# Performance work log

Hardware: AMD Instinct MI355X
Metric: run time of the kernel (lower is better)

Reference implementation:

```python
import jax, jax.numpy as jnp
import numpy as np

B, N, D_MODEL, HEADS, DFF, M = 4, 4096, 1024, 16, 4096, 256
DH = D_MODEL // HEADS  # 64
EPS_K = 1e-4
LN_EPS = 1e-5


def setup_inputs() -> dict:
    key = jax.random.key(0)
    ks = jax.random.split(key, 12)
    s = 0.02
    return {
        "video": jax.random.normal(ks[0], (B, N, D_MODEL), jnp.float32),
        "Wq": jax.random.normal(ks[1], (D_MODEL, D_MODEL), jnp.float32) * s,
        "bq": jnp.zeros((D_MODEL,), jnp.float32),
        "Wk": jax.random.normal(ks[2], (D_MODEL, D_MODEL), jnp.float32) * s,
        "bk": jnp.zeros((D_MODEL,), jnp.float32),
        "Wv": jax.random.normal(ks[3], (D_MODEL, D_MODEL), jnp.float32) * s,
        "bv": jnp.zeros((D_MODEL,), jnp.float32),
        "Wo": jax.random.normal(ks[4], (D_MODEL, D_MODEL), jnp.float32) * s,
        "bo": jnp.zeros((D_MODEL,), jnp.float32),
        "proj": jax.random.normal(ks[5], (M, DH), jnp.float32),  # random-feature matrix (buffer)
        "W1": jax.random.normal(ks[6], (DFF, D_MODEL), jnp.float32) * s,
        "b1": jnp.zeros((DFF,), jnp.float32),
        "W2": jax.random.normal(ks[7], (D_MODEL, DFF), jnp.float32) * s,
        "b2": jnp.zeros((D_MODEL,), jnp.float32),
        "g2": jnp.ones((D_MODEL,), jnp.float32),
        "be2": jnp.zeros((D_MODEL,), jnp.float32),
        "g3": jnp.ones((D_MODEL,), jnp.float32),
        "be3": jnp.zeros((D_MODEL,), jnp.float32),
    }


def softmax_kernel(x, proj, is_query):
    # FAVOR+ positive softmax random features (Performer).
    # x: [b,h,n,dh], proj: [m,dh]
    norm = x.shape[-1] ** -0.25  # data normalizer 1/d^{1/4}
    ratio = proj.shape[0] ** -0.5
    xp = jnp.einsum("bhnd,md->bhnm", x * norm, proj)
    diag = jnp.sum(jnp.square(x), axis=-1, keepdims=True) * 0.5 * (norm * norm)
    if is_query:
        stab = jnp.max(xp, axis=-1, keepdims=True)
    else:
        stab = jnp.max(xp, axis=(-1, -2), keepdims=True)
    return ratio * (jnp.exp(xp - diag - stab) + EPS_K)


def layer_norm(x, g, b):
    mu = jnp.mean(x, axis=-1, keepdims=True)
    var = jnp.mean(jnp.square(x - mu), axis=-1, keepdims=True)
    return (x - mu) * jax.lax.rsqrt(var + LN_EPS) * g + b


def reference(video, Wq, bq, Wk, bk, Wv, bv, Wo, bo, proj,
              W1, b1, W2, b2, g2, be2, g3, be3):
    b, n, d = video.shape
    split = lambda t: t.reshape(b, n, HEADS, DH).transpose(0, 2, 1, 3)  # [b,h,n,dh]
    q = split(video @ Wq.T + bq)
    k = split(video @ Wk.T + bk)
    v = split(video @ Wv.T + bv)

    qp = softmax_kernel(q, proj, is_query=True)   # [b,h,n,m]
    kp = softmax_kernel(k, proj, is_query=False)  # [b,h,n,m]

    # Non-causal linear attention: O(n*m*dh) instead of O(n^2)
    k_sum = jnp.sum(kp, axis=2)                              # [b,h,m]
    denom = jnp.einsum("bhnm,bhm->bhn", qp, k_sum)           # [b,h,n]
    ctx = jnp.einsum("bhnm,bhnd->bhmd", kp, v)               # [b,h,m,dh]
    out = jnp.einsum("bhnm,bhmd->bhnd", qp, ctx) / denom[..., None]

    attn = out.transpose(0, 2, 1, 3).reshape(b, n, d) @ Wo.T + bo
    x = layer_norm(video + attn, g2, be2)  # dropout is identity in eval
    ff = jax.nn.relu(x @ W1.T + b1) @ W2.T + b2
    return layer_norm(x + ff, g3, be3)
```

## Files before the change

### kernel.cpp

```cpp
#include <hip/hip_runtime.h>
#include <hip/hip_bf16.h>

#define N_TOK   4096
#define DMODEL  1024
#define NHEADS  16
#define DH      64
#define MFEAT   256
#define DFF     4096
#define BATCH   4
#define ROWS    (BATCH * N_TOK)

#define NORMF      0.35355339059327373f
#define HALF_NORM2 0.0625f
#define RATIO      0.0625f
#define EPSK       1e-4f
#define LNEPS      1e-5f

typedef unsigned short ushort_t;
using bfrag = __attribute__((ext_vector_type(8))) short;
using facc  = __attribute__((ext_vector_type(4))) float;
using ush8  = __attribute__((ext_vector_type(8))) unsigned short;

__device__ __forceinline__ float b2f(ushort_t u) {
    return __bfloat162float(__builtin_bit_cast(__hip_bfloat16, u));
}
__device__ __forceinline__ ushort_t f2b(float f) {
    return __builtin_bit_cast(ushort_t, __float2bfloat16(f));
}
__device__ __forceinline__ void stC(float* p, float v) { *p = v; }
__device__ __forceinline__ void stC(ushort_t* p, float v) { *p = f2b(v); }

__device__ __forceinline__ void gload_lds16(const void* g, void* l) {
    __builtin_amdgcn_global_load_lds(
        (const __attribute__((address_space(1))) unsigned int*)g,
        (__attribute__((address_space(3))) unsigned int*)l, 16, 0, 0);
}

template <int N>
__device__ __forceinline__ void waitcnt_vm() {
    if constexpr (N == 0)      asm volatile("s_waitcnt vmcnt(0)" ::: "memory");
    else if constexpr (N == 3) asm volatile("s_waitcnt vmcnt(3)" ::: "memory");
    else if constexpr (N == 4) asm volatile("s_waitcnt vmcnt(4)" ::: "memory");
    else if constexpr (N == 6) asm volatile("s_waitcnt vmcnt(6)" ::: "memory");
    else if constexpr (N == 8) asm volatile("s_waitcnt vmcnt(8)" ::: "memory");
}

__device__ __forceinline__ unsigned fkey(float f) {
    unsigned u = __float_as_uint(f);
    return (u & 0x80000000u) ? ~u : (u | 0x80000000u);
}
__device__ __forceinline__ float fdec(unsigned k) {
    return (k & 0x80000000u) ? __uint_as_float(k ^ 0x80000000u) : __uint_as_float(~k);
}

__global__ __launch_bounds__(256) void cvt_bf16(const float* __restrict__ s,
                                                ushort_t* __restrict__ d, int n4) {
    int i = blockIdx.x * 256 + threadIdx.x;
    if (i >= n4) return;
    float4 v = ((const float4*)s)[i];
    ((ushort4*)d)[i] = make_ushort4(f2b(v.x), f2b(v.y), f2b(v.z), f2b(v.w));
}

template <int FJ, typename OT>
__global__ __launch_bounds__(256) void gemm_mfma(
    const ushort_t* __restrict__ A, const ushort_t* __restrict__ W,
    const float* __restrict__ bias, OT* __restrict__ C,
    int Nout, int K, int relu)
{
    constexpr int BN = FJ * 32;
    constexpr int NLD = 2 + BN / 64;
    __shared__ short As[2][128 * 32];
    __shared__ short Ws[2][BN * 32];
    const int t = threadIdx.x;
    const unsigned nwg = gridDim.x * gridDim.y;
    const unsigned flat = blockIdx.y * gridDim.x + blockIdx.x;
    const unsigned cpx = nwg >> 3;
    const unsigned wg = (flat & 7) * cpx + (flat >> 3);
    const int m0 = (int)(wg / gridDim.x) * 128, n0 = (int)(wg % gridDim.x) * BN;
    const int lane = t & 63, wave = t >> 6;
    const int wr = (wave >> 1) * 64, wc = (wave & 1) * (FJ * 16);
    const int lm = lane & 15, kq = (lane >> 4) * 8;
    facc acc[4][FJ];
#pragma unroll
    for (int i = 0; i < 4; ++i)
#pragma unroll
        for (int j = 0; j < FJ; ++j) acc[i][j] = (facc){0.f, 0.f, 0.f, 0.f};

    auto stage = [&](int b, int k0) {
#pragma unroll
        for (int it = 0; it < 2; ++it) {
            int ch = t + it * 256;
            gload_lds16(A + (size_t)(m0 + (ch >> 2)) * K + k0 + (ch & 3) * 8, &As[b][ch * 8]);
        }
#pragma unroll
        for (int it = 0; it < BN / 64; ++it) {
            int ch = t + it * 256;
            gload_lds16(W + (size_t)(n0 + (ch >> 2)) * K + k0 + (ch & 3) * 8, &Ws[b][ch * 8]);
        }
    };
    auto compute = [&](int b) {
        bfrag af[4], bf[FJ];
#pragma unroll
        for (int i = 0; i < 4; ++i) af[i] = *(bfrag*)&As[b][(wr + i * 16 + lm) * 32 + kq];
#pragma unroll
        for (int j = 0; j < FJ; ++j) bf[j] = *(bfrag*)&Ws[b][(wc + j * 16 + lm) * 32 + kq];
#pragma unroll
        for (int i = 0; i < 4; ++i)
#pragma unroll
            for (int j = 0; j < FJ; ++j)
                acc[i][j] = __builtin_amdgcn_mfma_f32_16x16x32_bf16(af[i], bf[j], acc[i][j], 0, 0, 0);
    };

    stage(0, 0);
    int buf = 0;
    for (int k0 = 0; k0 < K - 32; k0 += 32) {
        stage(buf ^ 1, k0 + 32);
        waitcnt_vm<NLD>();
        __builtin_amdgcn_s_barrier();
        compute(buf);
        __builtin_amdgcn_s_barrier();
        buf ^= 1;
    }
    waitcnt_vm<0>();
    __builtin_amdgcn_s_barrier();
    compute(buf);

    const int rq = (lane >> 4) * 4;
#pragma unroll
    for (int i = 0; i < 4; ++i)
#pragma unroll
        for (int j = 0; j < FJ; ++j) {
            int col = n0 + wc + j * 16 + lm;
            float bc = bias[col];
#pragma unroll
            for (int r = 0; r < 4; ++r) {
                int row = m0 + wr + i * 16 + rq + r;
                float v = acc[i][j][r] + bc;
                if (relu) v = fmaxf(v, 0.f);
                stC(C + (size_t)row * Nout + col, v);
            }
        }
}

__global__ __launch_bounds__(256) void gemm_kv(
    const ushort_t* __restrict__ A,
    const ushort_t* __restrict__ WK, const ushort_t* __restrict__ WV,
    const float* __restrict__ bK, const float* __restrict__ bV,
    ushort_t* __restrict__ CK, ushort_t* __restrict__ CV)
{
    __shared__ short As[2][128 * 32];
    __shared__ short Ws[2][128 * 32];
    const int t = threadIdx.x;
    const unsigned nwg = gridDim.x * gridDim.y;
    const unsigned flat = blockIdx.y * gridDim.x + blockIdx.x;
    const unsigned cpx = nwg >> 3;
    const unsigned wg = (flat & 7) * cpx + (flat >> 3);
    const int m0 = (int)(wg / gridDim.x) * 128;
    const int nt = (int)(wg % gridDim.x);
    const ushort_t* W = (nt < 8) ? WK : WV;
    const float* bias = (nt < 8) ? bK : bV;
    ushort_t* C = (nt < 8) ? CK : CV;
    const int n0 = (nt & 7) * 128;
    const int lane = t & 63, wave = t >> 6;
    const int wr = (wave >> 1) * 64, wc = (wave & 1) * 64;
    const int lm = lane & 15, kq = (lane >> 4) * 8;
    facc acc[4][4];
#pragma unroll
    for (int i = 0; i < 4; ++i)
#pragma unroll
        for (int j = 0; j < 4; ++j) acc[i][j] = (facc){0.f, 0.f, 0.f, 0.f};

    auto stage = [&](int b, int k0) {
#pragma unroll
        for (int it = 0; it < 2; ++it) {
            int ch = t + it * 256;
            gload_lds16(A + (size_t)(m0 + (ch >> 2)) * DMODEL + k0 + (ch & 3) * 8, &As[b][ch * 8]);
            gload_lds16(W + (size_t)(n0 + (ch >> 2)) * DMODEL + k0 + (ch & 3) * 8, &Ws[b][ch * 8]);
        }
    };
    auto compute = [&](int b) {
        bfrag af[4], bf[4];
#pragma unroll
        for (int i = 0; i < 4; ++i) af[i] = *(bfrag*)&As[b][(wr + i * 16 + lm) * 32 + kq];
#pragma unroll
        for (int j = 0; j < 4; ++j) bf[j] = *(bfrag*)&Ws[b][(wc + j * 16 + lm) * 32 + kq];
#pragma unroll
        for (int i = 0; i < 4; ++i)
#pragma unroll
            for (int j = 0; j < 4; ++j)
                acc[i][j] = __builtin_amdgcn_mfma_f32_16x16x32_bf16(af[i], bf[j], acc[i][j], 0, 0, 0);
    };

    stage(0, 0);
    int buf = 0;
    for (int k0 = 0; k0 < DMODEL - 32; k0 += 32) {
        stage(buf ^ 1, k0 + 32);
        waitcnt_vm<4>();
        __builtin_amdgcn_s_barrier();
        compute(buf);
        __builtin_amdgcn_s_barrier();
        buf ^= 1;
    }
    waitcnt_vm<0>();
    __builtin_amdgcn_s_barrier();
    compute(buf);

    const int rq = (lane >> 4) * 4;
#pragma unroll
    for (int i = 0; i < 4; ++i)
#pragma unroll
        for (int j = 0; j < 4; ++j) {
            int col = n0 + wc + j * 16 + lm;
            float bc = bias[col];
#pragma unroll
            for (int r = 0; r < 4; ++r) {
                int row = m0 + wr + i * 16 + rq + r;
                C[(size_t)row * DMODEL + col] = f2b(acc[i][j][r] + bc);
            }
        }
}

__global__ __launch_bounds__(256) void vt_kernel(
    const ushort_t* __restrict__ V, ushort_t* __restrict__ VT)
{
    __shared__ ushort_t tile[64][68];
    const int t = threadIdx.x;
    const int n0 = blockIdx.x * 64, h = blockIdx.y;
#pragma unroll
    for (int i = 0; i < 4; ++i) {
        int idx = t + i * 256;
        int nl = idx >> 4, d4 = (idx & 15) * 4;
        ushort4 v = *(const ushort4*)(V + (size_t)(n0 + nl) * DMODEL + h * DH + d4);
        tile[nl][d4 + 0] = v.x; tile[nl][d4 + 1] = v.y;
        tile[nl][d4 + 2] = v.z; tile[nl][d4 + 3] = v.w;
    }
    __syncthreads();
#pragma unroll
    for (int i = 0; i < 4; ++i) {
        int idx = t + i * 256;
        int d = idx >> 4, n4 = (idx & 15) * 4;
        ushort4 o = make_ushort4(tile[n4][d], tile[n4 + 1][d], tile[n4 + 2][d], tile[n4 + 3][d]);
        *(ushort4*)(VT + (size_t)h * DH * N_TOK + (size_t)d * N_TOK + n0 + n4) = o;
    }
}

__global__ __launch_bounds__(256) void diagk_kernel(
    const ushort_t* __restrict__ Kb, float* __restrict__ diagK)
{
    const int lane = threadIdx.x & 63, wave = threadIdx.x >> 6;
    const int n = blockIdx.x * 4 + wave;
    const ushort_t* kr = Kb + (size_t)n * DMODEL + lane * 16;
    ush8 a = *(const ush8*)kr;
    ush8 b = *(const ush8*)(kr + 8);
    float s = 0.f;
#pragma unroll
    for (int e = 0; e < 8; ++e) { float x = b2f(a[e]); s += x * x; }
#pragma unroll
    for (int e = 0; e < 8; ++e) { float x = b2f(b[e]); s += x * x; }
    s += __shfl_xor(s, 1);
    s += __shfl_xor(s, 2);
    if ((lane & 3) == 0) diagK[(size_t)(lane >> 2) * N_TOK + n] = s;
}

__global__ __launch_bounds__(256) void xk_kernel(
    const ushort_t* __restrict__ projBF,
    const ushort_t* __restrict__ Kb,
    const float* __restrict__ diagK,
    unsigned* __restrict__ kmax16,
    ushort_t* __restrict__ KP,
    int mode)
{
    __shared__ short As[2][128 * 32];
    __shared__ short Ws[2][128 * 32];
    const int t = threadIdx.x;
    const int m0 = blockIdx.x * 128, n0 = blockIdx.y * 128, h = blockIdx.z;
    const ushort_t* Kh = Kb + h * DH;
    const int lane = t & 63, wave = t >> 6;
    const int wr = (wave >> 1) * 64, wc = (wave & 1) * 64;
    const int lm = lane & 15, kq = (lane >> 4) * 8;
    facc acc[4][4];
#pragma unroll
    for (int i = 0; i < 4; ++i)
#pragma unroll
        for (int j = 0; j < 4; ++j) acc[i][j] = (facc){0.f, 0.f, 0.f, 0.f};

    auto stage = [&](int b, int k0) {
#pragma unroll
        for (int it = 0; it < 2; ++it) {
            int ch = t + it * 256;
            gload_lds16(projBF + (size_t)(m0 + (ch >> 2)) * DH + k0 + (ch & 3) * 8, &As[b][ch * 8]);
            gload_lds16(Kh + (size_t)(n0 + (ch >> 2)) * DMODEL + k0 + (ch & 3) * 8, &Ws[b][ch * 8]);
        }
    };
    auto compute = [&](int b) {
        bfrag af[4], bf[4];
#pragma unroll
        for (int i = 0; i < 4; ++i) af[i] = *(bfrag*)&As[b][(wr + i * 16 + lm) * 32 + kq];
#pragma unroll
        for (int j = 0; j < 4; ++j) bf[j] = *(bfrag*)&Ws[b][(wc + j * 16 + lm) * 32 + kq];
#pragma unroll
        for (int i = 0; i < 4; ++i)
#pragma unroll
            for (int j = 0; j < 4; ++j)
                acc[i][j] = __builtin_amdgcn_mfma_f32_16x16x32_bf16(af[i], bf[j], acc[i][j], 0, 0, 0);
    };

    stage(0, 0);
    stage(1, 32);
    waitcnt_vm<4>();
    __builtin_amdgcn_s_barrier();
    compute(0);
    __builtin_amdgcn_s_barrier();
    waitcnt_vm<0>();
    __builtin_amdgcn_s_barrier();
    compute(1);

    const int rq = (lane >> 4) * 4;
    if (mode == 0) {
        float mx = -1e30f;
#pragma unroll
        for (int i = 0; i < 4; ++i)
#pragma unroll
            for (int j = 0; j < 4; ++j)
#pragma unroll
                for (int r = 0; r < 4; ++r) mx = fmaxf(mx, acc[i][j][r]);
        mx *= NORMF;
#pragma unroll
        for (int o = 32; o >= 1; o >>= 1) mx = fmaxf(mx, __shfl_xor(mx, o));
        if (lane == 0) atomicMax(kmax16 + h, fkey(mx));
    } else {
        const float stab = fdec(kmax16[h]);
        ushort_t* kb = KP + (size_t)h * MFEAT * N_TOK;
#pragma unroll
        for (int j = 0; j < 4; ++j) {
            int n = n0 + wc + j * 16 + lm;
            float dg = HALF_NORM2 * diagK[(size_t)h * N_TOK + n] + stab;
#pragma unroll
            for (int i = 0; i < 4; ++i)
#pragma unroll
                for (int r = 0; r < 4; ++r) {
                    int m = m0 + wr + i * 16 + rq + r;
                    float x = NORMF * acc[i][j][r];
                    kb[(size_t)m * N_TOK + n] = f2b(RATIO * (expf(x - dg) + EPSK));
                }
        }
    }
}

__global__ __launch_bounds__(256) void ksum_kernel(
    const ushort_t* __restrict__ KP, float* __restrict__ ksum)
{
    const int lane = threadIdx.x & 63, wave = threadIdx.x >> 6;
    const int row = blockIdx.x * 4 + wave;
    const ushort_t* kr = KP + (size_t)row * N_TOK;
    float s = 0.f;
#pragma unroll
    for (int it = 0; it < 8; ++it) {
        ush8 v = *(const ush8*)(kr + it * 512 + lane * 8);
#pragma unroll
        for (int e = 0; e < 8; ++e) s += b2f(v[e]);
    }
#pragma unroll
    for (int o = 32; o >= 1; o >>= 1) s += __shfl_xor(s, o);
    if (lane == 0) ksum[row] = s;
}

__global__ __launch_bounds__(256) void ctx_mfma(
    const ushort_t* __restrict__ KP, const ushort_t* __restrict__ VT,
    float* __restrict__ ctxp)
{
    __shared__ short As[2][128 * 32];
    __shared__ short Vs[2][64 * 32];
    const int t = threadIdx.x;
    const int z = blockIdx.x, mh = blockIdx.y, h = blockIdx.z;
    const ushort_t* A = KP + (size_t)h * MFEAT * N_TOK + (size_t)mh * 128 * N_TOK;
    const ushort_t* W = VT + (size_t)h * DH * N_TOK;
    const int lane = t & 63, wave = t >> 6;
    const int wr = (wave >> 1) * 64, wc = (wave & 1) * 32;
    const int lm = lane & 15, kq = (lane >> 4) * 8;
    facc acc[4][2];
#pragma unroll
    for (int i = 0; i < 4; ++i)
#pragma unroll
        for (int j = 0; j < 2; ++j) acc[i][j] = (facc){0.f, 0.f, 0.f, 0.f};

    auto stage = [&](int b, int k0) {
#pragma unroll
        for (int it = 0; it < 2; ++it) {
            int ch = t + it * 256;
            gload_lds16(A + (size_t)(ch >> 2) * N_TOK + k0 + (ch & 3) * 8, &As[b][ch * 8]);
        }
        gload_lds16(W + (size_t)(t >> 2) * N_TOK + k0 + (t & 3) * 8, &Vs[b][t * 8]);
    };
    auto compute = [&](int b) {
        bfrag af[4], bf[2];
#pragma unroll
        for (int i = 0; i < 4; ++i) af[i] = *(bfrag*)&As[b][(wr + i * 16 + lm) * 32 + kq];
#pragma unroll
        for (int j = 0; j < 2; ++j) bf[j] = *(bfrag*)&Vs[b][(wc + j * 16 + lm) * 32 + kq];
#pragma unroll
        for (int i = 0; i < 4; ++i)
#pragma unroll
            for (int j = 0; j < 2; ++j)
                acc[i][j] = __builtin_amdgcn_mfma_f32_16x16x32_bf16(af[i], bf[j], acc[i][j], 0, 0, 0);
    };

    const int kbeg = z * 512, kend = kbeg + 512;
    stage(0, kbeg);
    int buf = 0;
    for (int k0 = kbeg; k0 < kend - 32; k0 += 32) {
        stage(buf ^ 1, k0 + 32);
        waitcnt_vm<3>();
        __builtin_amdgcn_s_barrier();
        compute(buf);
        __builtin_amdgcn_s_barrier();
        buf ^= 1;
    }
    waitcnt_vm<0>();
    __builtin_amdgcn_s_barrier();
    compute(buf);

    const int rq = (lane >> 4) * 4;
    float* cb = ctxp + ((size_t)(z * NHEADS + h) * MFEAT + mh * 128) * DH;
#pragma unroll
    for (int i = 0; i < 4; ++i)
#pragma unroll
        for (int j = 0; j < 2; ++j)
#pragma unroll
            for (int r = 0; r < 4; ++r) {
                int m = wr + i * 16 + rq + r;
                int d = wc + j * 16 + lm;
                cb[(size_t)m * DH + d] = acc[i][j][r];
            }
}

__global__ __launch_bounds__(256) void ctx_transpose(
    const float* __restrict__ ctxp, ushort_t* __restrict__ ctxT)
{
    __shared__ float tile[64][65];
    const int h = blockIdx.x >> 2, mb = blockIdx.x & 3, t = threadIdx.x;
#pragma unroll
    for (int i = 0; i < 16; ++i) {
        int idx = t + i * 256;
        int ml = idx >> 6, d = idx & 63;
        int m = mb * 64 + ml;
        float s = 0.f;
#pragma unroll
        for (int z = 0; z < 8; ++z)
            s += ctxp[((size_t)(z * NHEADS + h) * MFEAT + m) * DH + d];
        tile[ml][d] = s;
    }
    __syncthreads();
    ushort_t* ob = ctxT + (size_t)h * DH * MFEAT;
#pragma unroll
    for (int i = 0; i < 16; ++i) {
        int idx = t + i * 256;
        int d = idx >> 6, ml = idx & 63;
        ob[(size_t)d * MFEAT + mb * 64 + ml] = f2b(tile[ml][d]);
    }
}

__global__ __launch_bounds__(256) void xp_gemm(
    const float* __restrict__ Q, const ushort_t* __restrict__ projBF,
    ushort_t* __restrict__ XP)
{
    __shared__ short As[128][40];
    __shared__ short Ws[128][40];
    const int t = threadIdx.x;
    const int m0 = blockIdx.x * 128, n0v = blockIdx.y * 128, h = blockIdx.z;
    const float* Qb = Q + h * DH;
    const int lane = t & 63, wave = t >> 6;
    const int wr = (wave >> 1) * 64, wc = (wave & 1) * 64;
    const int lm = lane & 15, kq = (lane >> 4) * 8;
    facc acc[4][4];
#pragma unroll
    for (int i = 0; i < 4; ++i)
#pragma unroll
        for (int j = 0; j < 4; ++j) acc[i][j] = (facc){0.f, 0.f, 0.f, 0.f};

    for (int k0 = 0; k0 < 64; k0 += 32) {
#pragma unroll
        for (int it = 0; it < 4; ++it) {
            int ch = t + it * 256;
            int row = ch >> 3, c4 = (ch & 7) * 4;
            float4 v = *(const float4*)(Qb + (size_t)(n0v + row) * DMODEL + k0 + c4);
            As[row][c4 + 0] = (short)f2b(v.x);
            As[row][c4 + 1] = (short)f2b(v.y);
            As[row][c4 + 2] = (short)f2b(v.z);
            As[row][c4 + 3] = (short)f2b(v.w);
        }
#pragma unroll
        for (int it = 0; it < 2; ++it) {
            int ch = t + it * 256;
            int row = ch >> 2, c8 = (ch & 3) * 8;
            *(uint4*)&Ws[row][c8] = *(const uint4*)(projBF + (size_t)(m0 + row) * DH + k0 + c8);
        }
        __syncthreads();
        bfrag af[4], bf[4];
#pragma unroll
        for (int i = 0; i < 4; ++i) af[i] = *(bfrag*)&As[wr + i * 16 + lm][kq];
#pragma unroll
        for (int j = 0; j < 4; ++j) bf[j] = *(bfrag*)&Ws[wc + j * 16 + lm][kq];
#pragma unroll
        for (int i = 0; i < 4; ++i)
#pragma unroll
            for (int j = 0; j < 4; ++j)
                acc[i][j] = __builtin_amdgcn_mfma_f32_16x16x32_bf16(af[i], bf[j], acc[i][j], 0, 0, 0);
        __syncthreads();
    }
    const int rq = (lane >> 4) * 4;
    ushort_t* xb = XP + (size_t)h * N_TOK * MFEAT;
#pragma unroll
    for (int i = 0; i < 4; ++i)
#pragma unroll
        for (int j = 0; j < 4; ++j) {
            int col = m0 + wc + j * 16 + lm;
#pragma unroll
            for (int r = 0; r < 4; ++r) {
                int row = n0v + wr + i * 16 + rq + r;
                xb[(size_t)row * MFEAT + col] = f2b(NORMF * acc[i][j][r]);
            }
        }
}

__global__ __launch_bounds__(256) void qp_kernel(
    ushort_t* __restrict__ XP, const float* __restrict__ Q,
    const float* __restrict__ ksum, float* __restrict__ denom)
{
    const int lane = threadIdx.x & 63, wave = threadIdx.x >> 6;
    const int row0 = (blockIdx.x * 4 + wave) * 8;
    for (int rr = 0; rr < 8; ++rr) {
        const int row = row0 + rr;
        const int h = row >> 12, n = row & 4095;
        ushort_t* xr = XP + (size_t)row * MFEAT + lane * 4;
        ushort4 xv = *(ushort4*)xr;
        float x0 = b2f(xv.x), x1 = b2f(xv.y), x2 = b2f(xv.z), x3 = b2f(xv.w);
        float qv = Q[(size_t)n * DMODEL + h * DH + lane];
        float ss = qv * qv;
#pragma unroll
        for (int o = 32; o >= 1; o >>= 1) ss += __shfl_xor(ss, o);
        float mx = fmaxf(fmaxf(x0, x1), fmaxf(x2, x3));
#pragma unroll
        for (int o = 32; o >= 1; o >>= 1) mx = fmaxf(mx, __shfl_xor(mx, o));
        const float sh = HALF_NORM2 * ss + mx;
        float p0 = RATIO * (expf(x0 - sh) + EPSK);
        float p1 = RATIO * (expf(x1 - sh) + EPSK);
        float p2 = RATIO * (expf(x2 - sh) + EPSK);
        float p3 = RATIO * (expf(x3 - sh) + EPSK);
        ushort4 pv = make_ushort4(f2b(p0), f2b(p1), f2b(p2), f2b(p3));
        *(ushort4*)xr = pv;
        float4 ks4 = *(const float4*)(ksum + h * MFEAT + lane * 4);
        float dn = b2f(pv.x) * ks4.x + b2f(pv.y) * ks4.y + b2f(pv.z) * ks4.z + b2f(pv.w) * ks4.w;
#pragma unroll
        for (int o = 32; o >= 1; o >>= 1) dn += __shfl_xor(dn, o);
        if (lane == 0) denom[row] = dn;
    }
}

__global__ __launch_bounds__(256) void out_gemm(
    const ushort_t* __restrict__ XP, const ushort_t* __restrict__ ctxT,
    const float* __restrict__ denom, ushort_t* __restrict__ OUT)
{
    __shared__ short As[2][128 * 32];
    __shared__ short Ws[2][64 * 32];
    const int t = threadIdx.x;
    const int n0 = blockIdx.x * 128, h = blockIdx.y;
    const ushort_t* A = XP + (size_t)h * N_TOK * MFEAT;
    const ushort_t* W = ctxT + (size_t)h * DH * MFEAT;
    const float* dnb = denom + (size_t)h * N_TOK;
    ushort_t* ob = OUT + h * DH;
    const int lane = t & 63, wave = t >> 6;
    const int wr = (wave >> 1) * 64, wc = (wave & 1) * 32;
    const int lm = lane & 15, kq = (lane >> 4) * 8;
    facc acc[4][2];
#pragma unroll
    for (int i = 0; i < 4; ++i)
#pragma unroll
        for (int j = 0; j < 2; ++j) acc[i][j] = (facc){0.f, 0.f, 0.f, 0.f};

    auto stage = [&](int b, int k0) {
#pragma unroll
        for (int it = 0; it < 2; ++it) {
            int ch = t + it * 256;
            gload_lds16(A + (size_t)(n0 + (ch >> 2)) * MFEAT + k0 + (ch & 3) * 8, &As[b][ch * 8]);
        }
        gload_lds16(W + (size_t)(t >> 2) * MFEAT + k0 + (t & 3) * 8, &Ws[b][t * 8]);
    };
    auto compute = [&](int b) {
        bfrag af[4], bf[2];
#pragma unroll
        for (int i = 0; i < 4; ++i) af[i] = *(bfrag*)&As[b][(wr + i * 16 + lm) * 32 + kq];
#pragma unroll
        for (int j = 0; j < 2; ++j) bf[j] = *(bfrag*)&Ws[b][(wc + j * 16 + lm) * 32 + kq];
#pragma unroll
        for (int i = 0; i < 4; ++i)
#pragma unroll
            for (int j = 0; j < 2; ++j)
                acc[i][j] = __builtin_amdgcn_mfma_f32_16x16x32_bf16(af[i], bf[j], acc[i][j], 0, 0, 0);
    };

    stage(0, 0);
    int buf = 0;
    for (int k0 = 0; k0 < MFEAT - 32; k0 += 32) {
        stage(buf ^ 1, k0 + 32);
        waitcnt_vm<3>();
        __builtin_amdgcn_s_barrier();
        compute(buf);
        __builtin_amdgcn_s_barrier();
        buf ^= 1;
    }
    waitcnt_vm<0>();
    __builtin_amdgcn_s_barrier();
    compute(buf);

    const int rq = (lane >> 4) * 4;
#pragma unroll
    for (int i = 0; i < 4; ++i)
#pragma unroll
        for (int r = 0; r < 4; ++r) {
            int row = n0 + wr + i * 16 + rq + r;
            float inv = 1.f / dnb[row];
#pragma unroll
            for (int j = 0; j < 2; ++j) {
                int col = wc + j * 16 + lm;
                ob[(size_t)row * DMODEL + col] = f2b(acc[i][j][r] * inv);
            }
        }
}

__global__ __launch_bounds__(256) void ln_kernel(
    const float* __restrict__ A, const void* __restrict__ Badd, int badd_bf16,
    const float* __restrict__ g, const float* __restrict__ bb,
    float* __restrict__ out, ushort_t* __restrict__ out_bf)
{
    __shared__ float red[8];
    const int row = blockIdx.x, t = threadIdx.x;
    const int lane = t & 63, wave = t >> 6;
    float4 av = ((const float4*)(A + (size_t)row * DMODEL))[t];
    float a0, a1, a2, a3;
    if (badd_bf16) {
        ushort4 bv4 = ((const ushort4*)Badd)[(size_t)row * (DMODEL / 4) + t];
        a0 = b2f(bv4.x); a1 = b2f(bv4.y); a2 = b2f(bv4.z); a3 = b2f(bv4.w);
    } else {
        float4 bf4 = ((const float4*)Badd)[(size_t)row * (DMODEL / 4) + t];
        a0 = bf4.x; a1 = bf4.y; a2 = bf4.z; a3 = bf4.w;
    }
    float v0 = av.x + a0, v1 = av.y + a1, v2 = av.z + a2, v3 = av.w + a3;
    float s = v0 + v1 + v2 + v3;
#pragma unroll
    for (int o = 32; o >= 1; o >>= 1) s += __shfl_xor(s, o);
    if (lane == 0) red[wave] = s;
    __syncthreads();
    float mu = (red[0] + red[1] + red[2] + red[3]) * (1.f / DMODEL);
    float d0 = v0 - mu, d1 = v1 - mu, d2 = v2 - mu, d3 = v3 - mu;
    float sq = d0 * d0 + d1 * d1 + d2 * d2 + d3 * d3;
#pragma unroll
    for (int o = 32; o >= 1; o >>= 1) sq += __shfl_xor(sq, o);
    if (lane == 0) red[4 + wave] = sq;
    __syncthreads();
    float rstd = rsqrtf((red[4] + red[5] + red[6] + red[7]) * (1.f / DMODEL) + LNEPS);
    float4 gv = ((const float4*)g)[t];
    float4 bv = ((const float4*)bb)[t];
    float o0 = d0 * rstd * gv.x + bv.x;
    float o1 = d1 * rstd * gv.y + bv.y;
    float o2 = d2 * rstd * gv.z + bv.z;
    float o3 = d3 * rstd * gv.w + bv.w;
    ((float4*)(out + (size_t)row * DMODEL))[t] = make_float4(o0, o1, o2, o3);
    if (out_bf)
        ((ushort4*)(out_bf + (size_t)row * DMODEL))[t] =
            make_ushort4(f2b(o0), f2b(o1), f2b(o2), f2b(o3));
}

extern "C" void kernel_launch(void* const* d_in, const int* in_sizes, int n_in,
                              void* d_out, int out_size, void* d_ws, size_t ws_size,
                              hipStream_t stream)
{
    const float* video = (const float*)d_in[0];
    const float* Wq = (const float*)d_in[1];
    const float* bq = (const float*)d_in[2];
    const float* Wk = (const float*)d_in[3];
    const float* bk = (const float*)d_in[4];
    const float* Wv = (const float*)d_in[5];
    const float* bv = (const float*)d_in[6];
    const float* Wo = (const float*)d_in[7];
    const float* bo = (const float*)d_in[8];
    const float* proj = (const float*)d_in[9];
    const float* W1 = (const float*)d_in[10];
    const float* b1 = (const float*)d_in[11];
    const float* W2 = (const float*)d_in[12];
    const float* b2 = (const float*)d_in[13];
    const float* g2 = (const float*)d_in[14];
    const float* be2 = (const float*)d_in[15];
    const float* g3 = (const float*)d_in[16];
    const float* be3 = (const float*)d_in[17];

    char* ws = (char*)d_ws;
    const size_t MB = 1048576ull;
    ushort_t* videoBF = (ushort_t*)(ws + 0);
    ushort_t* Kb   = (ushort_t*)(ws + 32 * MB);
    ushort_t* XBFb = (ushort_t*)(ws + 32 * MB);
    ushort_t* Vb   = (ushort_t*)(ws + 40 * MB);
    ushort_t* Fb   = (ushort_t*)(ws + 40 * MB);
    ushort_t* VTb  = (ushort_t*)(ws + 48 * MB);
    ushort_t* Yb   = (ushort_t*)(ws + 48 * MB);
    ushort_t* KP   = (ushort_t*)(ws + 56 * MB);
    ushort_t* Hb   = (ushort_t*)(ws + 56 * MB);
    ushort_t* ctxTb = (ushort_t*)(ws + 93847552ull + MB);
    char* smalls = ws + 91 * MB + 393216ull;
    float*    diagK  = (float*)(smalls);
    float*    ksum   = (float*)(smalls + 262144);
    float*    denomB = (float*)(smalls + 278528);
    unsigned* kmax16 = (unsigned*)(smalls + 540672);
    ushort_t* projBF = (ushort_t*)(smalls + 541184);
    float*    ctxp  = (float*)(ws + 92 * MB);
    ushort_t* OUTb = (ushort_t*)(ws + 92 * MB);
    ushort_t* WqBF = (ushort_t*)(ws + 100 * MB);
    ushort_t* WkBF = (ushort_t*)(ws + 102 * MB);
    ushort_t* WvBF = (ushort_t*)(ws + 104 * MB);
    ushort_t* WoBF = (ushort_t*)(ws + 106 * MB);
    ushort_t* W1BF = (ushort_t*)(ws + 108 * MB);
    ushort_t* W2BF = (ushort_t*)(ws + 116 * MB);
    float* Qbuf = (float*)d_out;

    dim3 blk(256);

    cvt_bf16<<<dim3(ROWS * DMODEL / 1024), blk, 0, stream>>>(video, videoBF, ROWS * DMODEL / 4);
    cvt_bf16<<<dim3(DMODEL * DMODEL / 1024), blk, 0, stream>>>(Wq, WqBF, DMODEL * DMODEL / 4);
    cvt_bf16<<<dim3(DMODEL * DMODEL / 1024), blk, 0, stream>>>(Wk, WkBF, DMODEL * DMODEL / 4);
    cvt_bf16<<<dim3(DMODEL * DMODEL / 1024), blk, 0, stream>>>(Wv, WvBF, DMODEL * DMODEL / 4);
    cvt_bf16<<<dim3(DMODEL * DMODEL / 1024), blk, 0, stream>>>(Wo, WoBF, DMODEL * DMODEL / 4);
    cvt_bf16<<<dim3(DFF * DMODEL / 1024), blk, 0, stream>>>(W1, W1BF, DFF * DMODEL / 4);
    cvt_bf16<<<dim3(DFF * DMODEL / 1024), blk, 0, stream>>>(W2, W2BF, DFF * DMODEL / 4);
    cvt_bf16<<<dim3(16), blk, 0, stream>>>(proj, projBF, MFEAT * DH / 4);

    gemm_mfma<4, float><<<dim3(8, ROWS / 128), blk, 0, stream>>>(
        videoBF, WqBF, bq, Qbuf, DMODEL, DMODEL, 0);

    dim3 gP(8, 32);

    for (int b = 0; b < BATCH; ++b) {
        const size_t roff = (size_t)b * N_TOK;
        const ushort_t* vbf = videoBF + roff * DMODEL;
        float* Qb = Qbuf + roff * DMODEL;

        gemm_kv<<<dim3(16, 32), blk, 0, stream>>>(vbf, WkBF, WvBF, bk, bv, Kb, Vb);
        vt_kernel<<<dim3(64, 16), blk, 0, stream>>>(Vb, VTb);
        diagk_kernel<<<dim3(1024), blk, 0, stream>>>(Kb, diagK);

        hipMemsetAsync(kmax16, 0, 64, stream);

        xk_kernel<<<dim3(2, 32, 16), blk, 0, stream>>>(projBF, Kb, diagK, kmax16, KP, 0);
        xk_kernel<<<dim3(2, 32, 16), blk, 0, stream>>>(projBF, Kb, diagK, kmax16, KP, 1);
        ksum_kernel<<<dim3(1024), blk, 0, stream>>>(KP, ksum);
        ctx_mfma<<<dim3(8, 2, 16), blk, 0, stream>>>(KP, VTb, ctxp);
        ctx_transpose<<<dim3(64), blk, 0, stream>>>(ctxp, ctxTb);

        xp_gemm<<<dim3(2, 32, 16), blk, 0, stream>>>(Qb, projBF, KP);
        qp_kernel<<<dim3(2048), blk, 0, stream>>>(KP, Qb, ksum, denomB);
        out_gemm<<<dim3(32, 16), blk, 0, stream>>>(KP, ctxTb, denomB, OUTb);

        gemm_mfma<4, ushort_t><<<gP, blk, 0, stream>>>(OUTb, WoBF, bo, Yb, DMODEL, DMODEL, 0);
        ln_kernel<<<dim3(N_TOK), blk, 0, stream>>>(
            video + roff * DMODEL, Yb, 1, g2, be2, Qb, XBFb);
        gemm_mfma<4, ushort_t><<<dim3(32, 32), blk, 0, stream>>>(
            XBFb, W1BF, b1, Hb, DFF, DMODEL, 1);
        gemm_mfma<2, ushort_t><<<dim3(16, 32), blk, 0, stream>>>(
            Hb, W2BF, b2, Fb, DMODEL, DFF, 0);
        ln_kernel<<<dim3(N_TOK), blk, 0, stream>>>(
            Qb, Fb, 1, g3, be3, Qb, nullptr);
    }
}
```

Baseline: 1.678 ms.

## Triple-buffer GEMM LDS stages, XOR-swizzle LDS layout, raise MFMA priority

All MFMA GEMM kernels move from double to triple LDS buffering. Each iteration now prefetches two steps ahead and keeps one barrier per step instead of two. Global-to-LDS chunk sources are XOR-swizzled by row, with fragment reads remapped to match, to cut LDS bank conflicts. MFMA blocks are wrapped in s_setprio to favour the matrix issue. The cost is more LDS per block, which may lower occupancy, and the single-barrier reuse relies on the three-buffer rotation staying correct.

```diff
diff --git a/kernel.cpp b/kernel.cpp
--- a/kernel.cpp
+++ b/kernel.cpp
@@ -53,6 +53,11 @@
     return (k & 0x80000000u) ? __uint_as_float(k ^ 0x80000000u) : __uint_as_float(~k);
 }
 
+__device__ __forceinline__ int src_c8(int ch) {
+    int row = ch >> 2;
+    return (((ch & 3) ^ (row & 3) ^ ((row >> 2) & 3)) * 8);
+}
+
 __global__ __launch_bounds__(256) void cvt_bf16(const float* __restrict__ s,
                                                 ushort_t* __restrict__ d, int n4) {
     int i = blockIdx.x * 256 + threadIdx.x;
@@ -69,8 +74,8 @@
 {
     constexpr int BN = FJ * 32;
     constexpr int NLD = 2 + BN / 64;
-    __shared__ short As[2][128 * 32];
-    __shared__ short Ws[2][BN * 32];
+    __shared__ short As[3][128 * 32];
+    __shared__ short Ws[3][BN * 32];
     const int t = threadIdx.x;
     const unsigned nwg = gridDim.x * gridDim.y;
     const unsigned flat = blockIdx.y * gridDim.x + blockIdx.x;
@@ -79,7 +84,8 @@
     const int m0 = (int)(wg / gridDim.x) * 128, n0 = (int)(wg % gridDim.x) * BN;
     const int lane = t & 63, wave = t >> 6;
     const int wr = (wave >> 1) * 64, wc = (wave & 1) * (FJ * 16);
-    const int lm = lane & 15, kq = (lane >> 4) * 8;
+    const int lm = lane & 15;
+    const int swl = ((lane >> 4) ^ (lm & 3) ^ ((lm >> 2) & 3)) * 8;
     facc acc[4][FJ];
 #pragma unroll
     for (int i = 0; i < 4; ++i)
@@ -90,40 +96,39 @@
 #pragma unroll
         for (int it = 0; it < 2; ++it) {
             int ch = t + it * 256;
-            gload_lds16(A + (size_t)(m0 + (ch >> 2)) * K + k0 + (ch & 3) * 8, &As[b][ch * 8]);
+            gload_lds16(A + (size_t)(m0 + (ch >> 2)) * K + k0 + src_c8(ch), &As[b][ch * 8]);
         }
 #pragma unroll
         for (int it = 0; it < BN / 64; ++it) {
             int ch = t + it * 256;
-            gload_lds16(W + (size_t)(n0 + (ch >> 2)) * K + k0 + (ch & 3) * 8, &Ws[b][ch * 8]);
+            gload_lds16(W + (size_t)(n0 + (ch >> 2)) * K + k0 + src_c8(ch), &Ws[b][ch * 8]);
         }
     };
     auto compute = [&](int b) {
         bfrag af[4], bf[FJ];
 #pragma unroll
-        for (int i = 0; i < 4; ++i) af[i] = *(bfrag*)&As[b][(wr + i * 16 + lm) * 32 + kq];
-#pragma unroll
-        for (int j = 0; j < FJ; ++j) bf[j] = *(bfrag*)&Ws[b][(wc + j * 16 + lm) * 32 + kq];
+        for (int i = 0; i < 4; ++i) af[i] = *(bfrag*)&As[b][(wr + i * 16 + lm) * 32 + swl];
+#pragma unroll
+        for (int j = 0; j < FJ; ++j) bf[j] = *(bfrag*)&Ws[b][(wc + j * 16 + lm) * 32 + swl];
+        __builtin_amdgcn_s_setprio(1);
 #pragma unroll
         for (int i = 0; i < 4; ++i)
 #pragma unroll
             for (int j = 0; j < FJ; ++j)
                 acc[i][j] = __builtin_amdgcn_mfma_f32_16x16x32_bf16(af[i], bf[j], acc[i][j], 0, 0, 0);
+        __builtin_amdgcn_s_setprio(0);
     };
 
     stage(0, 0);
-    int buf = 0;
-    for (int k0 = 0; k0 < K - 32; k0 += 32) {
-        stage(buf ^ 1, k0 + 32);
-        waitcnt_vm<NLD>();
+    stage(1, 32);
+    int buf = 0, stg = 2;
+    for (int k0 = 0; k0 < K; k0 += 32) {
+        if (k0 + 32 < K) waitcnt_vm<NLD>(); else waitcnt_vm<0>();
         __builtin_amdgcn_s_barrier();
+        if (k0 + 64 < K) { stage(stg, k0 + 64); stg = (stg == 2) ? 0 : stg + 1; }
         compute(buf);
-        __builtin_amdgcn_s_barrier();
-        buf ^= 1;
-    }
-    waitcnt_vm<0>();
-    __builtin_amdgcn_s_barrier();
-    compute(buf);
+        buf = (buf == 2) ? 0 : buf + 1;
+    }
 
     const int rq = (lane >> 4) * 4;
 #pragma unroll
@@ -148,8 +153,8 @@
     const float* __restrict__ bK, const float* __restrict__ bV,
     ushort_t* __restrict__ CK, ushort_t* __restrict__ CV)
 {
-    __shared__ short As[2][128 * 32];
-    __shared__ short Ws[2][128 * 32];
+    __shared__ short As[3][128 * 32];
+    __shared__ short Ws[3][128 * 32];
     const int t = threadIdx.x;
     const unsigned nwg = gridDim.x * gridDim.y;
     const unsigned flat = blockIdx.y * gridDim.x + blockIdx.x;
@@ -163,7 +168,8 @@
     const int n0 = (nt & 7) * 128;
     const int lane = t & 63, wave = t >> 6;
     const int wr = (wave >> 1) * 64, wc = (wave & 1) * 64;
-    const int lm = lane & 15, kq = (lane >> 4) * 8;
+    const int lm = lane & 15;
+    const int swl = ((lane >> 4) ^ (lm & 3) ^ ((lm >> 2) & 3)) * 8;
     facc acc[4][4];
 #pragma unroll
     for (int i = 0; i < 4; ++i)
@@ -174,36 +180,35 @@
 #pragma unroll
         for (int it = 0; it < 2; ++it) {
             int ch = t + it * 256;
-            gload_lds16(A + (size_t)(m0 + (ch >> 2)) * DMODEL + k0 + (ch & 3) * 8, &As[b][ch * 8]);
-            gload_lds16(W + (size_t)(n0 + (ch >> 2)) * DMODEL + k0 + (ch & 3) * 8, &Ws[b][ch * 8]);
+            gload_lds16(A + (size_t)(m0 + (ch >> 2)) * DMODEL + k0 + src_c8(ch), &As[b][ch * 8]);
+            gload_lds16(W + (size_t)(n0 + (ch >> 2)) * DMODEL + k0 + src_c8(ch), &Ws[b][ch * 8]);
         }
     };
     auto compute = [&](int b) {
         bfrag af[4], bf[4];
 #pragma unroll
-        for (int i = 0; i < 4; ++i) af[i] = *(bfrag*)&As[b][(wr + i * 16 + lm) * 32 + kq];
-#pragma unroll
-        for (int j = 0; j < 4; ++j) bf[j] = *(bfrag*)&Ws[b][(wc + j * 16 + lm) * 32 + kq];
+        for (int i = 0; i < 4; ++i) af[i] = *(bfrag*)&As[b][(wr + i * 16 + lm) * 32 + swl];
+#pragma unroll
+        for (int j = 0; j < 4; ++j) bf[j] = *(bfrag*)&Ws[b][(wc + j * 16 + lm) * 32 + swl];
+        __builtin_amdgcn_s_setprio(1);
 #pragma unroll
         for (int i = 0; i < 4; ++i)
 #pragma unroll
             for (int j = 0; j < 4; ++j)
                 acc[i][j] = __builtin_amdgcn_mfma_f32_16x16x32_bf16(af[i], bf[j], acc[i][j], 0, 0, 0);
+        __builtin_amdgcn_s_setprio(0);
     };
 
     stage(0, 0);
-    int buf = 0;
-    for (int k0 = 0; k0 < DMODEL - 32; k0 += 32) {
-        stage(buf ^ 1, k0 + 32);
-        waitcnt_vm<4>();
+    stage(1, 32);
+    int buf = 0, stg = 2;
+    for (int k0 = 0; k0 < DMODEL; k0 += 32) {
+        if (k0 + 32 < DMODEL) waitcnt_vm<4>(); else waitcnt_vm<0>();
         __builtin_amdgcn_s_barrier();
+        if (k0 + 64 < DMODEL) { stage(stg, k0 + 64); stg = (stg == 2) ? 0 : stg + 1; }
         compute(buf);
-        __builtin_amdgcn_s_barrier();
-        buf ^= 1;
-    }
-    waitcnt_vm<0>();
-    __builtin_amdgcn_s_barrier();
-    compute(buf);
+        buf = (buf == 2) ? 0 : buf + 1;
+    }
 
     const int rq = (lane >> 4) * 4;
 #pragma unroll
@@ -277,7 +282,8 @@
     const ushort_t* Kh = Kb + h * DH;
     const int lane = t & 63, wave = t >> 6;
     const int wr = (wave >> 1) * 64, wc = (wave & 1) * 64;
-    const int lm = lane & 15, kq = (lane >> 4) * 8;
+    const int lm = lane & 15;
+    const int swl = ((lane >> 4) ^ (lm & 3) ^ ((lm >> 2) & 3)) * 8;
     facc acc[4][4];
 #pragma unroll
     for (int i = 0; i < 4; ++i)
@@ -288,21 +294,23 @@
 #pragma unroll
         for (int it = 0; it < 2; ++it) {
             int ch = t + it * 256;
-            gload_lds16(projBF + (size_t)(m0 + (ch >> 2)) * DH + k0 + (ch & 3) * 8, &As[b][ch * 8]);
-            gload_lds16(Kh + (size_t)(n0 + (ch >> 2)) * DMODEL + k0 + (ch & 3) * 8, &Ws[b][ch * 8]);
+            gload_lds16(projBF + (size_t)(m0 + (ch >> 2)) * DH + k0 + src_c8(ch), &As[b][ch * 8]);
+            gload_lds16(Kh + (size_t)(n0 + (ch >> 2)) * DMODEL + k0 + src_c8(ch), &Ws[b][ch * 8]);
         }
     };
     auto compute = [&](int b) {
         bfrag af[4], bf[4];
 #pragma unroll
-        for (int i = 0; i < 4; ++i) af[i] = *(bfrag*)&As[b][(wr + i * 16 + lm) * 32 + kq];
-#pragma unroll
-        for (int j = 0; j < 4; ++j) bf[j] = *(bfrag*)&Ws[b][(wc + j * 16 + lm) * 32 + kq];
+        for (int i = 0; i < 4; ++i) af[i] = *(bfrag*)&As[b][(wr + i * 16 + lm) * 32 + swl];
+#pragma unroll
+        for (int j = 0; j < 4; ++j) bf[j] = *(bfrag*)&Ws[b][(wc + j * 16 + lm) * 32 + swl];
+        __builtin_amdgcn_s_setprio(1);
 #pragma unroll
         for (int i = 0; i < 4; ++i)
 #pragma unroll
             for (int j = 0; j < 4; ++j)
                 acc[i][j] = __builtin_amdgcn_mfma_f32_16x16x32_bf16(af[i], bf[j], acc[i][j], 0, 0, 0);
+        __builtin_amdgcn_s_setprio(0);
     };
 
     stage(0, 0);
@@ -310,7 +318,6 @@
     waitcnt_vm<4>();
     __builtin_amdgcn_s_barrier();
     compute(0);
-    __builtin_amdgcn_s_barrier();
     waitcnt_vm<0>();
     __builtin_amdgcn_s_barrier();
     compute(1);
@@ -369,15 +376,16 @@
     const ushort_t* __restrict__ KP, const ushort_t* __restrict__ VT,
     float* __restrict__ ctxp)
 {
-    __shared__ short As[2][128 * 32];
-    __shared__ short Vs[2][64 * 32];
+    __shared__ short As[3][128 * 32];
+    __shared__ short Vs[3][64 * 32];
     const int t = threadIdx.x;
     const int z = blockIdx.x, mh = blockIdx.y, h = blockIdx.z;
     const ushort_t* A = KP + (size_t)h * MFEAT * N_TOK + (size_t)mh * 128 * N_TOK;
     const ushort_t* W = VT + (size_t)h * DH * N_TOK;
     const int lane = t & 63, wave = t >> 6;
     const int wr = (wave >> 1) * 64, wc = (wave & 1) * 32;
-    const int lm = lane & 15, kq = (lane >> 4) * 8;
+    const int lm = lane & 15;
+    const int swl = ((lane >> 4) ^ (lm & 3) ^ ((lm >> 2) & 3)) * 8;
     facc acc[4][2];
 #pragma unroll
     for (int i = 0; i < 4; ++i)
@@ -388,37 +396,36 @@
 #pragma unroll
         for (int it = 0; it < 2; ++it) {
             int ch = t + it * 256;
-            gload_lds16(A + (size_t)(ch >> 2) * N_TOK + k0 + (ch & 3) * 8, &As[b][ch * 8]);
-        }
-        gload_lds16(W + (size_t)(t >> 2) * N_TOK + k0 + (t & 3) * 8, &Vs[b][t * 8]);
+            gload_lds16(A + (size_t)(ch >> 2) * N_TOK + k0 + src_c8(ch), &As[b][ch * 8]);
+        }
+        gload_lds16(W + (size_t)(t >> 2) * N_TOK + k0 + src_c8(t), &Vs[b][t * 8]);
     };
     auto compute = [&](int b) {
         bfrag af[4], bf[2];
 #pragma unroll
-        for (int i = 0; i < 4; ++i) af[i] = *(bfrag*)&As[b][(wr + i * 16 + lm) * 32 + kq];
-#pragma unroll
-        for (int j = 0; j < 2; ++j) bf[j] = *(bfrag*)&Vs[b][(wc + j * 16 + lm) * 32 + kq];
+        for (int i = 0; i < 4; ++i) af[i] = *(bfrag*)&As[b][(wr + i * 16 + lm) * 32 + swl];
+#pragma unroll
+        for (int j = 0; j < 2; ++j) bf[j] = *(bfrag*)&Vs[b][(wc + j * 16 + lm) * 32 + swl];
+        __builtin_amdgcn_s_setprio(1);
 #pragma unroll
         for (int i = 0; i < 4; ++i)
 #pragma unroll
             for (int j = 0; j < 2; ++j)
                 acc[i][j] = __builtin_amdgcn_mfma_f32_16x16x32_bf16(af[i], bf[j], acc[i][j], 0, 0, 0);
+        __builtin_amdgcn_s_setprio(0);
     };
 
     const int kbeg = z * 512, kend = kbeg + 512;
     stage(0, kbeg);
-    int buf = 0;
-    for (int k0 = kbeg; k0 < kend - 32; k0 += 32) {
-        stage(buf ^ 1, k0 + 32);
-        waitcnt_vm<3>();
+    stage(1, kbeg + 32);
+    int buf = 0, stg = 2;
+    for (int k0 = kbeg; k0 < kend; k0 += 32) {
+        if (k0 + 32 < kend) waitcnt_vm<3>(); else waitcnt_vm<0>();
         __builtin_amdgcn_s_barrier();
+        if (k0 + 64 < kend) { stage(stg, k0 + 64); stg = (stg == 2) ? 0 : stg + 1; }
         compute(buf);
-        __builtin_amdgcn_s_barrier();
-        buf ^= 1;
-    }
-    waitcnt_vm<0>();
-    __builtin_amdgcn_s_barrier();
-    compute(buf);
+        buf = (buf == 2) ? 0 : buf + 1;
+    }
 
     const int rq = (lane >> 4) * 4;
     float* cb = ctxp + ((size_t)(z * NHEADS + h) * MFEAT + mh * 128) * DH;
@@ -561,8 +568,8 @@
     const ushort_t* __restrict__ XP, const ushort_t* __restrict__ ctxT,
     const float* __restrict__ denom, ushort_t* __restrict__ OUT)
 {
-    __shared__ short As[2][128 * 32];
-    __shared__ short Ws[2][64 * 32];
+    __shared__ short As[3][128 * 32];
+    __shared__ short Ws[3][64 * 32];
     const int t = threadIdx.x;
     const int n0 = blockIdx.x * 128, h = blockIdx.y;
     const ushort_t* A = XP + (size_t)h * N_TOK * MFEAT;
@@ -571,7 +578,8 @@
     ushort_t* ob = OUT + h * DH;
     const int lane = t & 63, wave = t >> 6;
     const int wr = (wave >> 1) * 64, wc = (wave & 1) * 32;
-    const int lm = lane & 15, kq = (lane >> 4) * 8;
+    const int lm = lane & 15;
+    const int swl = ((lane >> 4) ^ (lm & 3) ^ ((lm >> 2) & 3)) * 8;
     facc acc[4][2];
 #pragma unroll
     for (int i = 0; i < 4; ++i)
@@ -582,36 +590,35 @@
 #pragma unroll
         for (int it = 0; it < 2; ++it) {
             int ch = t + it * 256;
-            gload_lds16(A + (size_t)(n0 + (ch >> 2)) * MFEAT + k0 + (ch & 3) * 8, &As[b][ch * 8]);
-        }
-        gload_lds16(W + (size_t)(t >> 2) * MFEAT + k0 + (t & 3) * 8, &Ws[b][t * 8]);
+            gload_lds16(A + (size_t)(n0 + (ch >> 2)) * MFEAT + k0 + src_c8(ch), &As[b][ch * 8]);
+        }
+        gload_lds16(W + (size_t)(t >> 2) * MFEAT + k0 + src_c8(t), &Ws[b][t * 8]);
     };
     auto compute = [&](int b) {
         bfrag af[4], bf[2];
 #pragma unroll
-        for (int i = 0; i < 4; ++i) af[i] = *(bfrag*)&As[b][(wr + i * 16 + lm) * 32 + kq];
-#pragma unroll
-        for (int j = 0; j < 2; ++j) bf[j] = *(bfrag*)&Ws[b][(wc + j * 16 + lm) * 32 + kq];
+        for (int i = 0; i < 4; ++i) af[i] = *(bfrag*)&As[b][(wr + i * 16 + lm) * 32 + swl];
+#pragma unroll
+        for (int j = 0; j < 2; ++j) bf[j] = *(bfrag*)&Ws[b][(wc + j * 16 + lm) * 32 + swl];
+        __builtin_amdgcn_s_setprio(1);
 #pragma unroll
         for (int i = 0; i < 4; ++i)
 #pragma unroll
             for (int j = 0; j < 2; ++j)
                 acc[i][j] = __builtin_amdgcn_mfma_f32_16x16x32_bf16(af[i], bf[j], acc[i][j], 0, 0, 0);
+        __builtin_amdgcn_s_setprio(0);
     };
 
     stage(0, 0);
-    int buf = 0;
-    for (int k0 = 0; k0 < MFEAT - 32; k0 += 32) {
-        stage(buf ^ 1, k0 + 32);
-        waitcnt_vm<3>();
+    stage(1, 32);
+    int buf = 0, stg = 2;
+    for (int k0 = 0; k0 < MFEAT; k0 += 32) {
+        if (k0 + 32 < MFEAT) waitcnt_vm<3>(); else waitcnt_vm<0>();
         __builtin_amdgcn_s_barrier();
+        if (k0 + 64 < MFEAT) { stage(stg, k0 + 64); stg = (stg == 2) ? 0 : stg + 1; }
         compute(buf);
-        __builtin_amdgcn_s_barrier();
-        buf ^= 1;
-    }
-    waitcnt_vm<0>();
-    __builtin_amdgcn_s_barrier();
-    compute(buf);
+        buf = (buf == 2) ? 0 : buf + 1;
+    }
 
     const int rq = (lane >> 4) * 4;
 #pragma unroll
```

Result: no change. 1.678 ms (-0.1%).
